# Kernel tuning notes

Measured on AMD Instinct MI355X. Metric: run time of the kernel, lower is better.

The kernel has to match this reference:

```python
import jax, jax.numpy as jnp
import numpy as np

DIM = 768
H = 12
HD = DIM // H
SCALE = HD ** (-0.5)


def setup_inputs() -> dict:
    key = jax.random.key(0)
    ks = jax.random.split(key, 10)
    s = DIM ** (-0.5)
    x = jax.random.normal(ks[0], (8, 1024, DIM), dtype=jnp.float32)
    Wq = jax.random.normal(ks[1], (DIM, DIM), dtype=jnp.float32) * s
    Wk = jax.random.normal(ks[2], (DIM, DIM), dtype=jnp.float32) * s
    Wv = jax.random.normal(ks[3], (DIM, DIM), dtype=jnp.float32) * s
    Wl = jax.random.normal(ks[4], (H, H), dtype=jnp.float32) * (H ** -0.5)
    bl = jax.random.normal(ks[5], (H,), dtype=jnp.float32) * 0.02
    Ww = jax.random.normal(ks[6], (H, H), dtype=jnp.float32) * (H ** -0.5)
    bw = jax.random.normal(ks[7], (H,), dtype=jnp.float32) * 0.02
    Wp = jax.random.normal(ks[8], (DIM, DIM), dtype=jnp.float32) * s
    bp = jax.random.normal(ks[9], (DIM,), dtype=jnp.float32) * 0.02
    return {"x": x, "Wq": Wq, "Wk": Wk, "Wv": Wv, "Wl": Wl, "bl": bl,
            "Ww": Ww, "bw": bw, "Wp": Wp, "bp": bp}


def reference(x, Wq, Wk, Wv, Wl, bl, Ww, bw, Wp, bp):
    B, N, C = x.shape
    # QKV projections (no bias), split heads -> (B, H, N, hd)
    q = (x @ Wq).reshape(B, N, H, HD).transpose(0, 2, 1, 3) * SCALE
    k = (x @ Wk).reshape(B, N, H, HD).transpose(0, 2, 1, 3)
    v = (x @ Wv).reshape(B, N, H, HD).transpose(0, 2, 1, 3)
    # scores: (B, H, N, N)
    attn = jnp.einsum('bhid,bhjd->bhij', q, k)
    # talking heads pre-softmax: mix over head axis (Linear on last dim of BNNH)
    attn = jnp.einsum('bhij,gh->bgij', attn, Wl) + bl[None, :, None, None]
    attn = jax.nn.softmax(attn, axis=-1)
    # talking heads post-softmax
    attn = jnp.einsum('bhij,gh->bgij', attn, Ww) + bw[None, :, None, None]
    out = jnp.einsum('bhij,bhjd->bhid', attn, v)  # (B, H, N, hd)
    out = out.transpose(0, 2, 1, 3).reshape(B, N, C)
    return out @ Wp + bp
```

## Files before the change

kernel.cpp:

```cpp
#include <hip/hip_runtime.h>
#include <hip/hip_bf16.h>

#define DIM 768
#define NH 12
#define HD 64
#define SEQ 1024
#define BATCH 8
#define LOG2E 1.44269504f

typedef __bf16 bf16x8 __attribute__((ext_vector_type(8)));
typedef _Float16 f16x4 __attribute__((ext_vector_type(4)));
typedef float f32x4 __attribute__((ext_vector_type(4)));

__global__ __launch_bounds__(256) void xcvt(
    const float* __restrict__ X, __bf16* __restrict__ Xb)
{
  const size_t i = ((size_t)blockIdx.x * 256 + threadIdx.x) * 8;
  float4 a0 = *(const float4*)(X + i);
  float4 a1 = *(const float4*)(X + i + 4);
  bf16x8 v = { (__bf16)a0.x, (__bf16)a0.y, (__bf16)a0.z, (__bf16)a0.w,
               (__bf16)a1.x, (__bf16)a1.y, (__bf16)a1.z, (__bf16)a1.w };
  *(bf16x8*)(Xb + i) = v;
}

__global__ __launch_bounds__(256) void wtrans(
    const float* __restrict__ Wq, const float* __restrict__ Wk,
    const float* __restrict__ Wv, const float* __restrict__ Wp,
    __bf16* __restrict__ Tq, __bf16* __restrict__ Tk,
    __bf16* __restrict__ Tv, __bf16* __restrict__ Tp)
{
  const int z = blockIdx.z;
  const float* W = (z==0) ? Wq : (z==1) ? Wk : (z==2) ? Wv : Wp;
  __bf16* T = (z==0) ? Tq : (z==1) ? Tk : (z==2) ? Tv : Tp;
  __shared__ float tile[32][33];
  const int t = threadIdx.x, tx = t & 31, ty = t >> 5;
  const int k0 = blockIdx.y * 32, n0 = blockIdx.x * 32;
#pragma unroll
  for (int u = 0; u < 4; ++u)
    tile[ty + u*8][tx] = W[(size_t)(k0 + ty + u*8) * DIM + n0 + tx];
  __syncthreads();
#pragma unroll
  for (int u = 0; u < 4; ++u)
    T[(size_t)(n0 + ty + u*8) * DIM + k0 + tx] = (__bf16)tile[tx][ty + u*8];
}

__global__ __launch_bounds__(256) void gemm_qkv(
    const __bf16* __restrict__ Xb, const __bf16* __restrict__ WT,
    __bf16* __restrict__ Qo, __bf16* __restrict__ Ko, _Float16* __restrict__ Vt2)
{
  __shared__ __bf16 As[128 * 40];
  __shared__ __bf16 Bs[128 * 40];

  const int t = threadIdx.x, lane = t & 63, w = t >> 6;
  const int n16 = lane & 15, q = lane >> 4;
  const int m0 = blockIdx.y * 128, n0 = blockIdx.x * 128;
  const int wm = (w >> 1) * 64, wn = (w & 1) * 64;

  const int srow = t >> 2, scol = (t & 3) * 8;
  const __bf16* Ag = Xb + (size_t)(m0 + srow) * DIM + scol;
  const __bf16* Bg = WT + (size_t)(n0 + srow) * DIM + scol;

  f32x4 acc[4][4];
#pragma unroll
  for (int mt = 0; mt < 4; ++mt)
#pragma unroll
    for (int nt = 0; nt < 4; ++nt) acc[mt][nt] = (f32x4){0.f,0.f,0.f,0.f};

  for (int kb = 0; kb < DIM; kb += 32) {
    __syncthreads();
    bf16x8 a0 = *(const bf16x8*)(Ag + kb);
    bf16x8 a1 = *(const bf16x8*)(Ag + (size_t)64 * DIM + kb);
    bf16x8 b0 = *(const bf16x8*)(Bg + kb);
    bf16x8 b1 = *(const bf16x8*)(Bg + (size_t)64 * DIM + kb);
    *(bf16x8*)&As[srow * 40 + scol] = a0;
    *(bf16x8*)&As[(srow + 64) * 40 + scol] = a1;
    *(bf16x8*)&Bs[srow * 40 + scol] = b0;
    *(bf16x8*)&Bs[(srow + 64) * 40 + scol] = b1;
    __syncthreads();

    bf16x8 af[4], bg[4];
#pragma unroll
    for (int mt = 0; mt < 4; ++mt)
      af[mt] = *(const bf16x8*)&As[(wm + mt*16 + n16) * 40 + q*8];
#pragma unroll
    for (int nt = 0; nt < 4; ++nt)
      bg[nt] = *(const bf16x8*)&Bs[(wn + nt*16 + n16) * 40 + q*8];
#pragma unroll
    for (int mt = 0; mt < 4; ++mt)
#pragma unroll
      for (int nt = 0; nt < 4; ++nt)
        acc[mt][nt] = __builtin_amdgcn_mfma_f32_16x16x32_bf16(af[mt], bg[nt], acc[mt][nt], 0, 0, 0);
  }

#pragma unroll
  for (int nt = 0; nt < 4; ++nt) {
    const int n = n0 + wn + nt*16 + n16;
    const int z = n / DIM, c = n % DIM;
    const int h = c >> 6, d = c & 63;
#pragma unroll
    for (int mt = 0; mt < 4; ++mt) {
#pragma unroll
      for (int r = 0; r < 4; ++r) {
        const int row = m0 + wm + mt*16 + q*4 + r;
        const int bb = row >> 10, ii = row & 1023;
        const float v = acc[mt][nt][r];
        if (z == 0)
          Qo[(((size_t)bb*NH + h)*SEQ + ii)*HD + d] = (__bf16)(v * 0.125f);
        else if (z == 1)
          Ko[(((size_t)bb*NH + h)*SEQ + ii)*HD + d] = (__bf16)v;
        else
          Vt2[((((size_t)bb*NH + h)*64 + (ii >> 4))*HD + d)*16 + (ii & 15)] = (_Float16)v;
      }
    }
  }
}

__global__ __launch_bounds__(256, 2) void attn_fused(
    const __bf16* __restrict__ Qg, const __bf16* __restrict__ Kg,
    const _Float16* __restrict__ Vt2,
    const float* __restrict__ Wl, const float* __restrict__ bl,
    const float* __restrict__ Ww, const float* __restrict__ bw,
    __bf16* __restrict__ Aout)
{
  __shared__ _Float16 Sl[2][12][324];
  __shared__ _Float16 Pl[2][16 * 248];

  const int t = threadIdx.x, lane = t & 63, w = t >> 6;
  const int n16 = lane & 15, q = lane >> 4;
  const int h0 = w * 3;
  const int b = blockIdx.x, i0 = blockIdx.y * 16;
  const size_t bbase = (size_t)b * NH * SEQ * HD;

  f16x4 wlA, wwA;
  f32x4 blC, bwC;
#pragma unroll
  for (int j = 0; j < 4; ++j) {
    const int k = q*4 + j;
    wlA[j] = (n16 < 12 && k < 12) ? (_Float16)(Wl[n16*12 + k] * LOG2E) : (_Float16)0.f;
    wwA[j] = (n16 < 12 && k < 12) ? (_Float16)Ww[n16*12 + k] : (_Float16)0.f;
    blC[j] = (k < 12) ? bl[k] * LOG2E : 0.f;
    bwC[j] = (k < 12) ? bw[k] : 0.f;
  }

  bf16x8 qf[3][2];
#pragma unroll
  for (int hh = 0; hh < 3; ++hh)
#pragma unroll
    for (int cc = 0; cc < 2; ++cc)
      qf[hh][cc] = *(const bf16x8*)(Qg + bbase + ((size_t)(h0+hh)*SEQ + i0 + n16)*HD + cc*32 + q*8);

  const f32x4 z4 = {0.f, 0.f, 0.f, 0.f};

  float lrun[4][4];
#pragma unroll
  for (int c = 0; c < 4; ++c)
#pragma unroll
    for (int r = 0; r < 4; ++r) lrun[c][r] = 0.f;

  bf16x8 kC[3][2], kN[3][2];
#pragma unroll
  for (int hh = 0; hh < 3; ++hh) {
    const __bf16* kp = Kg + bbase + ((size_t)(h0+hh)*SEQ + n16)*HD + q*8;
    kC[hh][0] = *(const bf16x8*)kp;
    kC[hh][1] = *(const bf16x8*)(kp + 32);
  }

#pragma unroll 2
  for (int jt = 0; jt < SEQ/16; ++jt) {
    const int buf = jt & 1;
    const int jn = (jt < SEQ/16 - 1) ? jt + 1 : jt;
#pragma unroll
    for (int hh = 0; hh < 3; ++hh) {
      const __bf16* kp = Kg + bbase + ((size_t)(h0+hh)*SEQ + jn*16 + n16)*HD + q*8;
      kN[hh][0] = *(const bf16x8*)kp;
      kN[hh][1] = *(const bf16x8*)(kp + 32);
    }
#pragma unroll
    for (int hh = 0; hh < 3; ++hh) {
      f32x4 s = __builtin_amdgcn_mfma_f32_16x16x32_bf16(kC[hh][0], qf[hh][0], z4, 0, 0, 0);
      s = __builtin_amdgcn_mfma_f32_16x16x32_bf16(kC[hh][1], qf[hh][1], s, 0, 0, 0);
      f16x4 sh = { (_Float16)s[0], (_Float16)s[1], (_Float16)s[2], (_Float16)s[3] };
      *(f16x4*)&Sl[buf][h0+hh][n16*20 + q*4] = sh;
    }
    __syncthreads();
#pragma unroll
    for (int c = 0; c < 4; ++c) {
      const int i = w*4 + c;
      f16x4 sf;
#pragma unroll
      for (int dd = 0; dd < 4; ++dd) {
        int h = q*4 + dd; if (h > 11) h = 11;
        sf[dd] = Sl[buf][h][i*20 + n16];
      }
      f32x4 sm = __builtin_amdgcn_mfma_f32_16x16x16f16(wlA, sf, blC, 0, 0, 0);
#pragma unroll
      for (int r = 0; r < 4; ++r) lrun[c][r] += __builtin_amdgcn_exp2f(sm[r]);
    }
#pragma unroll
    for (int hh = 0; hh < 3; ++hh) { kC[hh][0] = kN[hh][0]; kC[hh][1] = kN[hh][1]; }
  }

  float linv[4][4];
#pragma unroll
  for (int c = 0; c < 4; ++c)
#pragma unroll
    for (int r = 0; r < 4; ++r) {
      float l = lrun[c][r];
      l += __shfl_xor(l, 1);
      l += __shfl_xor(l, 2);
      l += __shfl_xor(l, 4);
      l += __shfl_xor(l, 8);
      linv[c][r] = 1.0f / l;
    }

  f32x4 oacc[3][4];
#pragma unroll
  for (int hh = 0; hh < 3; ++hh)
#pragma unroll
    for (int dc = 0; dc < 4; ++dc) oacc[hh][dc] = z4;

  f16x4 vC[3][4], vN[3][4];
#pragma unroll
  for (int hh = 0; hh < 3; ++hh) {
    const __bf16* kp = Kg + bbase + ((size_t)(h0+hh)*SEQ + n16)*HD + q*8;
    kC[hh][0] = *(const bf16x8*)kp;
    kC[hh][1] = *(const bf16x8*)(kp + 32);
  }

#pragma unroll 2
  for (int jt = 0; jt < SEQ/16; ++jt) {
    const int buf = jt & 1;
    const int jn = (jt < SEQ/16 - 1) ? jt + 1 : jt;
#pragma unroll
    for (int hh = 0; hh < 3; ++hh) {
      const __bf16* kp = Kg + bbase + ((size_t)(h0+hh)*SEQ + jn*16 + n16)*HD + q*8;
      kN[hh][0] = *(const bf16x8*)kp;
      kN[hh][1] = *(const bf16x8*)(kp + 32);
    }
#pragma unroll
    for (int hh = 0; hh < 3; ++hh) {
      const _Float16* vb = Vt2 + (((size_t)(b*NH + h0 + hh)*64 + jt)*HD)*16;
#pragma unroll
      for (int dc = 0; dc < 4; ++dc)
        vN[hh][dc] = *(const f16x4*)(vb + (size_t)(dc*16 + n16)*16 + q*4);
    }
#pragma unroll
    for (int hh = 0; hh < 3; ++hh) {
      f32x4 s = __builtin_amdgcn_mfma_f32_16x16x32_bf16(kC[hh][0], qf[hh][0], z4, 0, 0, 0);
      s = __builtin_amdgcn_mfma_f32_16x16x32_bf16(kC[hh][1], qf[hh][1], s, 0, 0, 0);
      f16x4 sh = { (_Float16)s[0], (_Float16)s[1], (_Float16)s[2], (_Float16)s[3] };
      *(f16x4*)&Sl[buf][h0+hh][n16*20 + q*4] = sh;
    }
    __syncthreads();
#pragma unroll
    for (int c = 0; c < 4; ++c) {
      const int i = w*4 + c;
      f16x4 sf;
#pragma unroll
      for (int dd = 0; dd < 4; ++dd) {
        int h = q*4 + dd; if (h > 11) h = 11;
        sf[dd] = Sl[buf][h][i*20 + n16];
      }
      f32x4 sm = __builtin_amdgcn_mfma_f32_16x16x16f16(wlA, sf, blC, 0, 0, 0);
      f16x4 pnf;
#pragma unroll
      for (int r = 0; r < 4; ++r)
        pnf[r] = (_Float16)(__builtin_amdgcn_exp2f(sm[r]) * linv[c][r]);
      f32x4 p2 = __builtin_amdgcn_mfma_f32_16x16x16f16(wwA, pnf, bwC, 0, 0, 0);
      if (q < 3) {
#pragma unroll
        for (int r = 0; r < 4; ++r)
          Pl[buf][i*248 + (q*4 + r)*20 + n16] = (_Float16)p2[r];
      }
    }
    if (jt > 0) {
#pragma unroll
      for (int hh = 0; hh < 3; ++hh) {
        const int g2 = h0 + hh;
        f16x4 pa = *(const f16x4*)&Pl[1 - buf][n16*248 + g2*20 + q*4];
#pragma unroll
        for (int dc = 0; dc < 4; ++dc)
          oacc[hh][dc] = __builtin_amdgcn_mfma_f32_16x16x16f16(pa, vC[hh][dc], oacc[hh][dc], 0, 0, 0);
      }
    }
#pragma unroll
    for (int hh = 0; hh < 3; ++hh) {
      kC[hh][0] = kN[hh][0]; kC[hh][1] = kN[hh][1];
#pragma unroll
      for (int dc = 0; dc < 4; ++dc) vC[hh][dc] = vN[hh][dc];
    }
  }
  __syncthreads();
#pragma unroll
  for (int hh = 0; hh < 3; ++hh) {
    const int g2 = h0 + hh;
    f16x4 pa = *(const f16x4*)&Pl[1][n16*248 + g2*20 + q*4];
#pragma unroll
    for (int dc = 0; dc < 4; ++dc)
      oacc[hh][dc] = __builtin_amdgcn_mfma_f32_16x16x16f16(pa, vC[hh][dc], oacc[hh][dc], 0, 0, 0);
  }

#pragma unroll
  for (int hh = 0; hh < 3; ++hh)
#pragma unroll
    for (int dc = 0; dc < 4; ++dc)
#pragma unroll
      for (int r = 0; r < 4; ++r)
        Aout[((size_t)(b*SEQ + i0 + q*4 + r))*DIM + (h0+hh)*HD + dc*16 + n16] =
            (__bf16)oacc[hh][dc][r];
}

__global__ __launch_bounds__(256) void gemm_proj(
    const __bf16* __restrict__ A, const __bf16* __restrict__ WpT,
    const float* __restrict__ bp, float* __restrict__ Out)
{
  __shared__ __bf16 As[128 * 40];
  __shared__ __bf16 Bs[128 * 40];

  const int t = threadIdx.x, lane = t & 63, w = t >> 6;
  const int n16 = lane & 15, q = lane >> 4;
  const int m0 = blockIdx.y * 128, n0 = blockIdx.x * 128;
  const int wm = (w >> 1) * 64, wn = (w & 1) * 64;

  const int srow = t >> 2, scol = (t & 3) * 8;
  const __bf16* Ag = A + (size_t)(m0 + srow) * DIM + scol;
  const __bf16* Bg = WpT + (size_t)(n0 + srow) * DIM + scol;

  f32x4 acc[4][4];
#pragma unroll
  for (int nt = 0; nt < 4; ++nt) {
    const float bpv = bp[n0 + wn + nt*16 + n16];
#pragma unroll
    for (int mt = 0; mt < 4; ++mt)
#pragma unroll
      for (int r = 0; r < 4; ++r) acc[mt][nt][r] = bpv;
  }

  for (int kb = 0; kb < DIM; kb += 32) {
    __syncthreads();
    bf16x8 a0 = *(const bf16x8*)(Ag + kb);
    bf16x8 a1 = *(const bf16x8*)(Ag + (size_t)64 * DIM + kb);
    bf16x8 b0 = *(const bf16x8*)(Bg + kb);
    bf16x8 b1 = *(const bf16x8*)(Bg + (size_t)64 * DIM + kb);
    *(bf16x8*)&As[srow * 40 + scol] = a0;
    *(bf16x8*)&As[(srow + 64) * 40 + scol] = a1;
    *(bf16x8*)&Bs[srow * 40 + scol] = b0;
    *(bf16x8*)&Bs[(srow + 64) * 40 + scol] = b1;
    __syncthreads();

    bf16x8 af[4], bg[4];
#pragma unroll
    for (int mt = 0; mt < 4; ++mt)
      af[mt] = *(const bf16x8*)&As[(wm + mt*16 + n16) * 40 + q*8];
#pragma unroll
    for (int nt = 0; nt < 4; ++nt)
      bg[nt] = *(const bf16x8*)&Bs[(wn + nt*16 + n16) * 40 + q*8];
#pragma unroll
    for (int mt = 0; mt < 4; ++mt)
#pragma unroll
      for (int nt = 0; nt < 4; ++nt)
        acc[mt][nt] = __builtin_amdgcn_mfma_f32_16x16x32_bf16(af[mt], bg[nt], acc[mt][nt], 0, 0, 0);
  }

#pragma unroll
  for (int nt = 0; nt < 4; ++nt) {
    const int n = n0 + wn + nt*16 + n16;
#pragma unroll
    for (int mt = 0; mt < 4; ++mt)
#pragma unroll
      for (int r = 0; r < 4; ++r) {
        const int row = m0 + wm + mt*16 + q*4 + r;
        Out[(size_t)row * DIM + n] = acc[mt][nt][r];
      }
  }
}

extern "C" void kernel_launch(void* const* d_in, const int* in_sizes, int n_in,
                              void* d_out, int out_size, void* d_ws, size_t ws_size,
                              hipStream_t stream) {
  const float* x  = (const float*)d_in[0];
  const float* Wq = (const float*)d_in[1];
  const float* Wk = (const float*)d_in[2];
  const float* Wv = (const float*)d_in[3];
  const float* Wl = (const float*)d_in[4];
  const float* bl = (const float*)d_in[5];
  const float* Ww = (const float*)d_in[6];
  const float* bw = (const float*)d_in[7];
  const float* Wp = (const float*)d_in[8];
  const float* bp = (const float*)d_in[9];

  char* p = (char*)d_ws;
  const size_t WSZ = (size_t)DIM * DIM * 2;
  const size_t TSZ = (size_t)BATCH * NH * SEQ * HD * 2;
  __bf16*   WqT = (__bf16*)p;            p += WSZ;
  __bf16*   WkT = (__bf16*)p;            p += WSZ;
  __bf16*   WvT = (__bf16*)p;            p += WSZ;
  __bf16*   WpT = (__bf16*)p;            p += WSZ;
  __bf16*   Q   = (__bf16*)p;            p += TSZ;
  __bf16*   K   = (__bf16*)p;            p += TSZ;
  _Float16* V2  = (_Float16*)p;          p += TSZ;
  __bf16*   AO  = (__bf16*)p;            p += TSZ;
  __bf16*   Xb  = (__bf16*)p;            p += TSZ;

  xcvt<<<dim3((BATCH*SEQ*DIM)/(256*8)), 256, 0, stream>>>(x, Xb);
  wtrans<<<dim3(24, 24, 4), 256, 0, stream>>>(Wq, Wk, Wv, Wp, WqT, WkT, WvT, WpT);
  gemm_qkv<<<dim3(18, 64), 256, 0, stream>>>(Xb, WqT, Q, K, V2);
  attn_fused<<<dim3(BATCH, SEQ/16), 256, 0, stream>>>(Q, K, V2, Wl, bl, Ww, bw, AO);
  gemm_proj<<<dim3(6, 64), 256, 0, stream>>>(AO, WpT, bp, (float*)d_out);
}
```

Baseline: 435.3 us.

## Use direct global-to-LDS loads in GEMMs and reorder attention PV MFMAs with priority

The QKV and projection GEMMs now stage tiles through global_load_lds (16-byte direct loads into LDS) in place of register round-trips, and the LDS padding is dropped to fit the wave-contiguous layout. In the attention kernel, the P·V MFMA block moves ahead of the softmax/talking-heads section, and s_setprio raises wave priority around MFMA bursts to improve interleaving across waves. The aim is to cut VGPR traffic and issue overhead in the GEMMs and to overlap matrix work with the exp/LDS phases in attention. Removing the padding may bring back LDS bank conflicts on the fragment reads. Missing waitcnt handling for the asynchronous LDS loads could also be a correctness risk.

Result: faster. 422.9 us (-2.9%).

```diff
diff --git a/kernel.cpp b/kernel.cpp
--- a/kernel.cpp
+++ b/kernel.cpp
@@ -11,6 +11,12 @@
 typedef __bf16 bf16x8 __attribute__((ext_vector_type(8)));
 typedef _Float16 f16x4 __attribute__((ext_vector_type(4)));
 typedef float f32x4 __attribute__((ext_vector_type(4)));
+
+__device__ __forceinline__ void gload_lds16(const __bf16* g, __bf16* l) {
+  __builtin_amdgcn_global_load_lds(
+      (const __attribute__((address_space(1))) void*)g,
+      (__attribute__((address_space(3))) void*)l, 16, 0, 0);
+}
 
 __global__ __launch_bounds__(256) void xcvt(
     const float* __restrict__ X, __bf16* __restrict__ Xb)
@@ -48,8 +54,8 @@
     const __bf16* __restrict__ Xb, const __bf16* __restrict__ WT,
     __bf16* __restrict__ Qo, __bf16* __restrict__ Ko, _Float16* __restrict__ Vt2)
 {
-  __shared__ __bf16 As[128 * 40];
-  __shared__ __bf16 Bs[128 * 40];
+  __shared__ __bf16 As[128 * 32];
+  __shared__ __bf16 Bs[128 * 32];
 
   const int t = threadIdx.x, lane = t & 63, w = t >> 6;
   const int n16 = lane & 15, q = lane >> 4;
@@ -59,6 +65,10 @@
   const int srow = t >> 2, scol = (t & 3) * 8;
   const __bf16* Ag = Xb + (size_t)(m0 + srow) * DIM + scol;
   const __bf16* Bg = WT + (size_t)(n0 + srow) * DIM + scol;
+  __bf16* AsW0 = &As[w * 512];
+  __bf16* AsW1 = &As[2048 + w * 512];
+  __bf16* BsW0 = &Bs[w * 512];
+  __bf16* BsW1 = &Bs[2048 + w * 512];
 
   f32x4 acc[4][4];
 #pragma unroll
@@ -68,23 +78,19 @@
 
   for (int kb = 0; kb < DIM; kb += 32) {
     __syncthreads();
-    bf16x8 a0 = *(const bf16x8*)(Ag + kb);
-    bf16x8 a1 = *(const bf16x8*)(Ag + (size_t)64 * DIM + kb);
-    bf16x8 b0 = *(const bf16x8*)(Bg + kb);
-    bf16x8 b1 = *(const bf16x8*)(Bg + (size_t)64 * DIM + kb);
-    *(bf16x8*)&As[srow * 40 + scol] = a0;
-    *(bf16x8*)&As[(srow + 64) * 40 + scol] = a1;
-    *(bf16x8*)&Bs[srow * 40 + scol] = b0;
-    *(bf16x8*)&Bs[(srow + 64) * 40 + scol] = b1;
+    gload_lds16(Ag + kb, AsW0);
+    gload_lds16(Ag + (size_t)64 * DIM + kb, AsW1);
+    gload_lds16(Bg + kb, BsW0);
+    gload_lds16(Bg + (size_t)64 * DIM + kb, BsW1);
     __syncthreads();
 
     bf16x8 af[4], bg[4];
 #pragma unroll
     for (int mt = 0; mt < 4; ++mt)
-      af[mt] = *(const bf16x8*)&As[(wm + mt*16 + n16) * 40 + q*8];
+      af[mt] = *(const bf16x8*)&As[(wm + mt*16 + n16) * 32 + q*8];
 #pragma unroll
     for (int nt = 0; nt < 4; ++nt)
-      bg[nt] = *(const bf16x8*)&Bs[(wn + nt*16 + n16) * 40 + q*8];
+      bg[nt] = *(const bf16x8*)&Bs[(wn + nt*16 + n16) * 32 + q*8];
 #pragma unroll
     for (int mt = 0; mt < 4; ++mt)
 #pragma unroll
@@ -175,6 +181,7 @@
       kN[hh][0] = *(const bf16x8*)kp;
       kN[hh][1] = *(const bf16x8*)(kp + 32);
     }
+    __builtin_amdgcn_s_setprio(1);
 #pragma unroll
     for (int hh = 0; hh < 3; ++hh) {
       f32x4 s = __builtin_amdgcn_mfma_f32_16x16x32_bf16(kC[hh][0], qf[hh][0], z4, 0, 0, 0);
@@ -182,6 +189,7 @@
       f16x4 sh = { (_Float16)s[0], (_Float16)s[1], (_Float16)s[2], (_Float16)s[3] };
       *(f16x4*)&Sl[buf][h0+hh][n16*20 + q*4] = sh;
     }
+    __builtin_amdgcn_s_setprio(0);
     __syncthreads();
 #pragma unroll
     for (int c = 0; c < 4; ++c) {
@@ -244,6 +252,7 @@
       for (int dc = 0; dc < 4; ++dc)
         vN[hh][dc] = *(const f16x4*)(vb + (size_t)(dc*16 + n16)*16 + q*4);
     }
+    __builtin_amdgcn_s_setprio(1);
 #pragma unroll
     for (int hh = 0; hh < 3; ++hh) {
       f32x4 s = __builtin_amdgcn_mfma_f32_16x16x32_bf16(kC[hh][0], qf[hh][0], z4, 0, 0, 0);
@@ -251,7 +260,21 @@
       f16x4 sh = { (_Float16)s[0], (_Float16)s[1], (_Float16)s[2], (_Float16)s[3] };
       *(f16x4*)&Sl[buf][h0+hh][n16*20 + q*4] = sh;
     }
-    __syncthreads();
+    __builtin_amdgcn_s_setprio(0);
+    __syncthreads();
+    if (jt > 0) {
+      f16x4 pa[3];
+#pragma unroll
+      for (int hh = 0; hh < 3; ++hh)
+        pa[hh] = *(const f16x4*)&Pl[1 - buf][n16*248 + (h0+hh)*20 + q*4];
+      __builtin_amdgcn_s_setprio(1);
+#pragma unroll
+      for (int hh = 0; hh < 3; ++hh)
+#pragma unroll
+        for (int dc = 0; dc < 4; ++dc)
+          oacc[hh][dc] = __builtin_amdgcn_mfma_f32_16x16x16f16(pa[hh], vC[hh][dc], oacc[hh][dc], 0, 0, 0);
+      __builtin_amdgcn_s_setprio(0);
+    }
 #pragma unroll
     for (int c = 0; c < 4; ++c) {
       const int i = w*4 + c;
@@ -273,16 +296,6 @@
           Pl[buf][i*248 + (q*4 + r)*20 + n16] = (_Float16)p2[r];
       }
     }
-    if (jt > 0) {
-#pragma unroll
-      for (int hh = 0; hh < 3; ++hh) {
-        const int g2 = h0 + hh;
-        f16x4 pa = *(const f16x4*)&Pl[1 - buf][n16*248 + g2*20 + q*4];
-#pragma unroll
-        for (int dc = 0; dc < 4; ++dc)
-          oacc[hh][dc] = __builtin_amdgcn_mfma_f32_16x16x16f16(pa, vC[hh][dc], oacc[hh][dc], 0, 0, 0);
-      }
-    }
 #pragma unroll
     for (int hh = 0; hh < 3; ++hh) {
       kC[hh][0] = kN[hh][0]; kC[hh][1] = kN[hh][1];
@@ -314,8 +327,8 @@
     const __bf16* __restrict__ A, const __bf16* __restrict__ WpT,
     const float* __restrict__ bp, float* __restrict__ Out)
 {
-  __shared__ __bf16 As[128 * 40];
-  __shared__ __bf16 Bs[128 * 40];
+  __shared__ __bf16 As[128 * 32];
+  __shared__ __bf16 Bs[128 * 32];
 
   const int t = threadIdx.x, lane = t & 63, w = t >> 6;
   const int n16 = lane & 15, q = lane >> 4;
@@ -325,6 +338,10 @@
   const int srow = t >> 2, scol = (t & 3) * 8;
   const __bf16* Ag = A + (size_t)(m0 + srow) * DIM + scol;
   const __bf16* Bg = WpT + (size_t)(n0 + srow) * DIM + scol;
+  __bf16* AsW0 = &As[w * 512];
+  __bf16* AsW1 = &As[2048 + w * 512];
+  __bf16* BsW0 = &Bs[w * 512];
+  __bf16* BsW1 = &Bs[2048 + w * 512];
 
   f32x4 acc[4][4];
 #pragma unroll
@@ -338,23 +355,19 @@
 
   for (int kb = 0; kb < DIM; kb += 32) {
     __syncthreads();
-    bf16x8 a0 = *(const bf16x8*)(Ag + kb);
-    bf16x8 a1 = *(const bf16x8*)(Ag + (size_t)64 * DIM + kb);
-    bf16x8 b0 = *(const bf16x8*)(Bg + kb);
-    bf16x8 b1 = *(const bf16x8*)(Bg + (size_t)64 * DIM + kb);
-    *(bf16x8*)&As[srow * 40 + scol] = a0;
-    *(bf16x8*)&As[(srow + 64) * 40 + scol] = a1;
-    *(bf16x8*)&Bs[srow * 40 + scol] = b0;
-    *(bf16x8*)&Bs[(srow + 64) * 40 + scol] = b1;
+    gload_lds16(Ag + kb, AsW0);
+    gload_lds16(Ag + (size_t)64 * DIM + kb, AsW1);
+    gload_lds16(Bg + kb, BsW0);
+    gload_lds16(Bg + (size_t)64 * DIM + kb, BsW1);
     __syncthreads();
 
     bf16x8 af[4], bg[4];
 #pragma unroll
     for (int mt = 0; mt < 4; ++mt)
-      af[mt] = *(const bf16x8*)&As[(wm + mt*16 + n16) * 40 + q*8];
+      af[mt] = *(const bf16x8*)&As[(wm + mt*16 + n16) * 32 + q*8];
 #pragma unroll
     for (int nt = 0; nt < 4; ++nt)
-      bg[nt] = *(const bf16x8*)&Bs[(wn + nt*16 + n16) * 40 + q*8];
+      bg[nt] = *(const bf16x8*)&Bs[(wn + nt*16 + n16) * 32 + q*8];
 #pragma unroll
     for (int mt = 0; mt < 4; ++mt)
 #pragma unroll
```
